# Optimization experiments

Measured on AMD Instinct MI355X. Metric: run time of the kernel, lower is better.

The kernel has to match this reference:

```python
import jax, jax.numpy as jnp
import numpy as np

B, T, N, D_IN = 2, 64, 64, 512
HID, L, H = 256, 2, 4
C = HID // H  # 64 per-head channels
NEG_SLOPE = 0.2
LN_EPS = 1e-5


def setup_inputs() -> dict:
    key = jax.random.key(0)
    ks = jax.random.split(key, 8)
    s_in = 1.0 / np.sqrt(D_IN)
    s_h = 1.0 / np.sqrt(HID)
    s_c = 1.0 / np.sqrt(C)
    return {
        "x": jax.random.normal(ks[0], (B, T, N, D_IN), jnp.float32),
        "person_mask": jax.random.randint(ks[1], (B, T, N), 0, 2) > 0,
        "W_in": (jax.random.normal(ks[2], (D_IN, HID)) * s_in).astype(jnp.float32),
        "b_in": jnp.zeros((HID,), jnp.float32),
        "Wl": (jax.random.normal(ks[3], (L, HID, HID)) * s_h).astype(jnp.float32),
        "bl": jnp.zeros((L, HID), jnp.float32),
        "Wr": (jax.random.normal(ks[4], (L, HID, HID)) * s_h).astype(jnp.float32),
        "br": jnp.zeros((L, HID), jnp.float32),
        "att": (jax.random.normal(ks[5], (L, H, C)) * s_c).astype(jnp.float32),
        "out_bias": jnp.zeros((L, HID), jnp.float32),
        "ln_scale": jnp.ones((L, HID), jnp.float32),
        "ln_bias": jnp.zeros((L, HID), jnp.float32),
    }


def _layernorm(x, g, b):
    mu = jnp.mean(x, axis=-1, keepdims=True)
    var = jnp.mean(jnp.square(x - mu), axis=-1, keepdims=True)
    return (x - mu) * jax.lax.rsqrt(var + LN_EPS) * g + b


def _gatv2_layer(h, allowed, Wl, bl, Wr, br, att, ob):
    # h: [bt, N, HID]; allowed: [bt, N, N] bool (edge j->i at [b,i,j])
    bt, n, _ = h.shape
    xl = (h @ Wl + bl).reshape(bt, n, H, C)  # source features (messages)
    xr = (h @ Wr + br).reshape(bt, n, H, C)  # target features
    # GATv2 logit: e_ij = a . leaky_relu(xr_i + xl_j), per head
    s = xr[:, :, None, :, :] + xl[:, None, :, :, :]  # [bt, i, j, H, C]
    e = jnp.einsum('bijhc,hc->bijh', jax.nn.leaky_relu(s, NEG_SLOPE), att)
    e = jnp.where(allowed[..., None], e, -1e9)
    alpha = jax.nn.softmax(e, axis=2)  # segment softmax over incoming edges j
    out = jnp.einsum('bijh,bjhc->bihc', alpha, xl)  # weighted scatter-sum
    return out.reshape(bt, n, H * C) + ob


def _forward(x, person_mask, W_in, b_in, Wl, bl, Wr, br, att, out_bias, ln_scale, ln_bias):
    b, t, n, _ = x.shape
    bt = b * t
    h = (x @ W_in + b_in).reshape(bt, n, HID)
    m = person_mask.reshape(bt, n)
    # edges: all pairs among masked nodes (incl. diag) + self loops for every node
    allowed = (m[:, :, None] & m[:, None, :]) | jnp.eye(n, dtype=bool)[None]
    hi = h
    for li in range(L):
        res = hi
        g = _gatv2_layer(hi, allowed, Wl[li], bl[li], Wr[li], br[li], att[li], out_bias[li])
        g = jax.nn.elu(g)  # dropout is identity in eval mode
        g = _layernorm(g, ln_scale[li], ln_bias[li])
        hi = g + res  # use_residual=True
        hi = jnp.where(m[:, :, None], hi, 0.0)
    # graphs with <=1 masked node are skipped (pass through projected features)
    keep = (jnp.sum(m, axis=-1) > 1)[:, None, None]
    out = jnp.where(keep, hi, h)
    return out.reshape(b, t, n, HID)


def reference(x, person_mask, W_in, b_in, Wl, bl, Wr, br, att, out_bias, ln_scale, ln_bias):
    return _forward(x, person_mask, W_in, b_in, Wl, bl, Wr, br, att, out_bias, ln_scale, ln_bias)
```

## Files before the change

### kernel.cpp

```cpp
#include <hip/hip_runtime.h>
#include <hip/hip_bf16.h>

#define BT_G   128
#define NND    64
#define D_IN_  512
#define HID_   256
#define NH     4
#define NCH    64
#define NROWS  8192
#define LN_EPS_    1e-5f

typedef __hip_bfloat16 bf16;
typedef __attribute__((ext_vector_type(8))) short short8;
typedef __attribute__((ext_vector_type(4))) float float4v;

__device__ __forceinline__ float toF(bf16 x) { return __bfloat162float(x); }

__global__ __launch_bounds__(256) void transpose_all_kernel(
    const float* __restrict__ W_in, const float* __restrict__ Wl,
    const float* __restrict__ Wr, const unsigned int* __restrict__ mw,
    bf16* __restrict__ WTin, bf16* __restrict__ WlrT, int* __restrict__ mout) {
    const int z = blockIdx.z;
    const int tid = threadIdx.x;
    if (z == 5) {
        if (blockIdx.x || blockIdx.y) return;
        __shared__ int okInt, okF32, okB16, okByte;
        if (tid == 0) { okInt = 1; okF32 = 1; okB16 = 1; okByte = 1; }
        __syncthreads();
        int aI = 1, aF = 1, aB = 1, aC = 1;
        for (int i = tid; i < 2048; i += 256) {
            unsigned w = mw[i];
            aI &= (w <= 1u);
            aF &= (w == 0u || w == 0x3F800000u);
            unsigned lo = w & 0xFFFFu, hi = w >> 16;
            aB &= ((lo == 0u || lo == 0x3F80u) && (hi == 0u || hi == 0x3F80u));
            aC &= (((w | (w >> 8) | (w >> 16) | (w >> 24)) & 0xFEu) == 0u);
        }
        if (!aI) atomicAnd(&okInt, 0);
        if (!aF) atomicAnd(&okF32, 0);
        if (!aB) atomicAnd(&okB16, 0);
        if (!aC) atomicAnd(&okByte, 0);
        __syncthreads();
        const int layout = (okInt || okF32) ? 0 : (okB16 ? 2 : (okByte ? 3 : 0));
        for (int i = tid; i < NROWS; i += 256) {
            int v;
            if (layout == 2)      v = (((const unsigned short*)mw)[i] != 0);
            else if (layout == 3) v = (((const unsigned char*)mw)[i] != 0);
            else                  v = (mw[i] != 0u);
            mout[i] = v;
        }
        return;
    }
    __shared__ float t[32][33];
    const float* src; bf16* dst; int K;
    if (z == 0)      { src = W_in;                 dst = WTin;                    K = 512; }
    else if (z <= 2) { src = Wl + (z - 1) * 65536; dst = WlrT + (z - 1) * 131072; K = 256; }
    else             { src = Wr + (z - 3) * 65536; dst = WlrT + (z - 3) * 131072 + 256 * 256; K = 256; }
    const int n0 = blockIdx.x * 32, k0 = blockIdx.y * 32;
    if (k0 >= K) return;
    const int tx = tid & 31, ty = tid >> 5;
    #pragma unroll
    for (int i = 0; i < 4; ++i)
        t[ty + 8 * i][tx] = src[(size_t)(k0 + ty + 8 * i) * 256 + n0 + tx];
    __syncthreads();
    #pragma unroll
    for (int i = 0; i < 4; ++i)
        dst[(size_t)(n0 + ty + 8 * i) * K + k0 + tx] =
            __float2bfloat16(t[tx][ty + 8 * i]);
}

__global__ __launch_bounds__(256) void gemm_in_kernel(
    const float* __restrict__ A, const bf16* __restrict__ BT,
    const float* __restrict__ bias, float* __restrict__ Cf,
    bf16* __restrict__ Cb16)
{
    __shared__ bf16 As[64 * 72];
    __shared__ bf16 Bs[64 * 72];
    const int tid  = threadIdx.x;
    const int wave = tid >> 6, lane = tid & 63;
    const int quad = lane >> 4, l16 = lane & 15;
    const int m0 = blockIdx.y * 64, n0 = blockIdx.x * 64;
    const int wm = (wave & 1) * 32, wn = (wave >> 1) * 32;
    float4v acc[2][2] = {};
    const int r  = tid >> 2;
    const int cq = (tid & 3) * 16;

    for (int k0 = 0; k0 < D_IN_; k0 += 64) {
        const float* sa = A + (size_t)(m0 + r) * D_IN_ + k0 + cq;
        const float4 f0 = *(const float4*)(sa);
        const float4 f1 = *(const float4*)(sa + 4);
        const float4 f2 = *(const float4*)(sa + 8);
        const float4 f3 = *(const float4*)(sa + 12);
        const bf16* sb = BT + (size_t)(n0 + r) * D_IN_ + k0 + cq;
        const float4 b0 = *(const float4*)(sb);
        const float4 b1 = *(const float4*)(sb + 8);
        union { bf16 h[16]; float4 v[2]; } u;
        u.h[0]=__float2bfloat16(f0.x); u.h[1]=__float2bfloat16(f0.y);
        u.h[2]=__float2bfloat16(f0.z); u.h[3]=__float2bfloat16(f0.w);
        u.h[4]=__float2bfloat16(f1.x); u.h[5]=__float2bfloat16(f1.y);
        u.h[6]=__float2bfloat16(f1.z); u.h[7]=__float2bfloat16(f1.w);
        u.h[8]=__float2bfloat16(f2.x); u.h[9]=__float2bfloat16(f2.y);
        u.h[10]=__float2bfloat16(f2.z); u.h[11]=__float2bfloat16(f2.w);
        u.h[12]=__float2bfloat16(f3.x); u.h[13]=__float2bfloat16(f3.y);
        u.h[14]=__float2bfloat16(f3.z); u.h[15]=__float2bfloat16(f3.w);
        __syncthreads();
        *(float4*)(&As[r * 72 + cq])     = u.v[0];
        *(float4*)(&As[r * 72 + cq + 8]) = u.v[1];
        *(float4*)(&Bs[r * 72 + cq])     = b0;
        *(float4*)(&Bs[r * 72 + cq + 8]) = b1;
        __syncthreads();
        #pragma unroll
        for (int kk = 0; kk < 64; kk += 32) {
            short8 af[2], bf2[2];
            #pragma unroll
            for (int mi = 0; mi < 2; ++mi)
                af[mi] = *(const short8*)(&As[(wm + mi * 16 + l16) * 72 + kk + quad * 8]);
            #pragma unroll
            for (int ni = 0; ni < 2; ++ni)
                bf2[ni] = *(const short8*)(&Bs[(wn + ni * 16 + l16) * 72 + kk + quad * 8]);
            #pragma unroll
            for (int mi = 0; mi < 2; ++mi)
                #pragma unroll
                for (int ni = 0; ni < 2; ++ni)
                    acc[mi][ni] = __builtin_amdgcn_mfma_f32_16x16x32_bf16(
                        af[mi], bf2[ni], acc[mi][ni], 0, 0, 0);
        }
    }
    #pragma unroll
    for (int ni = 0; ni < 2; ++ni) {
        const int col = n0 + wn + ni * 16 + l16;
        const float bv = bias[col];
        #pragma unroll
        for (int mi = 0; mi < 2; ++mi)
            #pragma unroll
            for (int rr = 0; rr < 4; ++rr) {
                const int row = m0 + wm + mi * 16 + quad * 4 + rr;
                const float v = acc[mi][ni][rr] + bv;
                Cf[(size_t)row * HID_ + col] = v;
                Cb16[(size_t)row * HID_ + col] = __float2bfloat16(v);
            }
    }
}

__global__ __launch_bounds__(256) void gemm_mfma_kernel(
    const bf16* __restrict__ A, const bf16* __restrict__ BT,
    const float* __restrict__ bias0, const float* __restrict__ bias1,
    float* __restrict__ Ca, float* __restrict__ Cbf, int M, int K)
{
    __shared__ bf16 As[128 * 72];
    __shared__ bf16 Bs[64 * 72];
    const int tid  = threadIdx.x;
    const int wave = tid >> 6, lane = tid & 63;
    const int quad = lane >> 4, l16 = lane & 15;
    const int m0 = blockIdx.y * 128, n0g = blockIdx.x * 64;
    const int wm = (wave & 1) * 64, wn = (wave >> 1) * 32;
    float4v acc[4][2] = {};
    const int r  = tid >> 2;
    const int cq = (tid & 3) * 16;

    for (int k0 = 0; k0 < K; k0 += 64) {
        const bf16* sa0 = A  + (size_t)(m0 + r) * K + k0 + cq;
        const bf16* sa1 = sa0 + (size_t)64 * K;
        const bf16* sb  = BT + (size_t)(n0g + r) * K + k0 + cq;
        const float4 a00 = *(const float4*)(sa0);
        const float4 a01 = *(const float4*)(sa0 + 8);
        const float4 a10 = *(const float4*)(sa1);
        const float4 a11 = *(const float4*)(sa1 + 8);
        const float4 b0  = *(const float4*)(sb);
        const float4 b1  = *(const float4*)(sb + 8);
        __syncthreads();
        *(float4*)(&As[r * 72 + cq])            = a00;
        *(float4*)(&As[r * 72 + cq + 8])        = a01;
        *(float4*)(&As[(r + 64) * 72 + cq])     = a10;
        *(float4*)(&As[(r + 64) * 72 + cq + 8]) = a11;
        *(float4*)(&Bs[r * 72 + cq])            = b0;
        *(float4*)(&Bs[r * 72 + cq + 8])        = b1;
        __syncthreads();
        #pragma unroll
        for (int kk = 0; kk < 64; kk += 32) {
            short8 af[4], bf2[2];
            #pragma unroll
            for (int mi = 0; mi < 4; ++mi)
                af[mi] = *(const short8*)(&As[(wm + mi * 16 + l16) * 72 + kk + quad * 8]);
            #pragma unroll
            for (int ni = 0; ni < 2; ++ni)
                bf2[ni] = *(const short8*)(&Bs[(wn + ni * 16 + l16) * 72 + kk + quad * 8]);
            #pragma unroll
            for (int mi = 0; mi < 4; ++mi)
                #pragma unroll
                for (int ni = 0; ni < 2; ++ni)
                    acc[mi][ni] = __builtin_amdgcn_mfma_f32_16x16x32_bf16(
                        af[mi], bf2[ni], acc[mi][ni], 0, 0, 0);
        }
    }
    const bool loHalf = (n0g < 256);
    float* Co = loHalf ? Ca : Cbf;
    const float* bp = loHalf ? bias0 : bias1;
    const int cbase = loHalf ? n0g : (n0g - 256);
    #pragma unroll
    for (int ni = 0; ni < 2; ++ni) {
        const int col = cbase + wn + ni * 16 + l16;
        const float bv = bp[col];
        #pragma unroll
        for (int mi = 0; mi < 4; ++mi)
            #pragma unroll
            for (int rr = 0; rr < 4; ++rr) {
                const int row = m0 + wm + mi * 16 + quad * 4 + rr;
                Co[(size_t)row * 256 + col] = acc[mi][ni][rr] + bv;
            }
    }
}

__global__ __launch_bounds__(256) void attn_kernel(
    const float* xl, const float* xr, const float* att,
    const int* msk, float* g)
{
    __shared__ float xls [64][68];
    __shared__ float xlsT[64][68];
    __shared__ float xrsT[64][68];
    __shared__ float esT [64][68];
    __shared__ float av[64], P[64], Q[64], mxf[64], inv[64];
    __shared__ float pmax[4][64], psum[4][64];
    __shared__ int   ms[64];
    const int tid  = threadIdx.x;
    const int head = blockIdx.x, gr = blockIdx.y;
    const int ti = tid >> 4, tj = tid & 15;
    const int i0 = ti * 4, j0 = tj * 4;
    const float* xlg = xl + (size_t)gr * NND * HID_ + head * NCH;
    const float* xrg = xr + (size_t)gr * NND * HID_ + head * NCH;

    {
        const int r  = tid >> 2;
        const int c0 = (tid & 3) * 16;
        float a[4][4], b[4][4];
        #pragma unroll
        for (int k = 0; k < 4; ++k) {
            *(float4*)a[k] = *(const float4*)(xlg + r * HID_ + c0 + 4 * k);
            *(float4*)b[k] = *(const float4*)(xrg + r * HID_ + c0 + 4 * k);
        }
        #pragma unroll
        for (int k = 0; k < 4; ++k)
            *(float4*)&xls[r][c0 + 4 * k] = *(float4*)a[k];
        #pragma unroll
        for (int k = 0; k < 4; ++k)
            #pragma unroll
            for (int w = 0; w < 4; ++w) {
                xlsT[c0 + 4 * k + w][r] = a[k][w];
                xrsT[c0 + 4 * k + w][r] = b[k][w];
            }
    }
    if (tid < 64) {
        av[tid] = att[head * NCH + tid];
        ms[tid] = msk[gr * NND + tid];
    }
    __syncthreads();

    float aa[4][4] = {};
    for (int c = 0; c < 64; ++c) {
        float xr4[4], xl4[4];
        *(float4*)xr4 = *(const float4*)&xrsT[c][i0];
        *(float4*)xl4 = *(const float4*)&xlsT[c][j0];
        const float a = av[c];
        #pragma unroll
        for (int y = 0; y < 4; ++y)
            #pragma unroll
            for (int x = 0; x < 4; ++x)
                aa[y][x] = fmaf(a, fabsf(xr4[y] + xl4[x]), aa[y][x]);
    }
    if (tid < 64) {
        float s = 0.f;
        for (int c = 0; c < 64; ++c) s = fmaf(av[c], xrsT[c][tid], s);
        P[tid] = s;
    } else if (tid < 128) {
        const int j = tid - 64;
        float s = 0.f;
        for (int c = 0; c < 64; ++c) s = fmaf(av[c], xlsT[c][j], s);
        Q[j] = s;
    }
    __syncthreads();

    {
        float Pv[4], Qv[4]; int mi4[4], mj4[4];
        #pragma unroll
        for (int y = 0; y < 4; ++y) { Pv[y] = P[i0 + y]; mi4[y] = ms[i0 + y]; }
        #pragma unroll
        for (int x = 0; x < 4; ++x) { Qv[x] = Q[j0 + x]; mj4[x] = ms[j0 + x]; }
        #pragma unroll
        for (int x = 0; x < 4; ++x) {
            float col[4];
            #pragma unroll
            for (int y = 0; y < 4; ++y) {
                float e = fmaf(0.4f, aa[y][x], 0.6f * (Pv[y] + Qv[x]));
                const bool allowed = (mi4[y] && mj4[x]) || (i0 + y == j0 + x);
                col[y] = allowed ? e : -1e9f;
            }
            *(float4*)&esT[j0 + x][i0] = *(float4*)col;
        }
    }
    __syncthreads();

    {
        const int si = tid & 63, q = tid >> 6;
        float mx = -1e30f;
        #pragma unroll
        for (int k = 0; k < 16; ++k) mx = fmaxf(mx, esT[16 * q + k][si]);
        pmax[q][si] = mx;
    }
    __syncthreads();
    if (tid < 64)
        mxf[tid] = fmaxf(fmaxf(pmax[0][tid], pmax[1][tid]),
                         fmaxf(pmax[2][tid], pmax[3][tid]));
    __syncthreads();
    {
        const int si = tid & 63, q = tid >> 6;
        const float mx = mxf[si];
        float s = 0.f;
        #pragma unroll
        for (int k = 0; k < 16; ++k) {
            const float ev = __expf(esT[16 * q + k][si] - mx);
            esT[16 * q + k][si] = ev;
            s += ev;
        }
        psum[q][si] = s;
    }
    __syncthreads();
    if (tid < 64)
        inv[tid] = 1.f / (psum[0][tid] + psum[1][tid] + psum[2][tid] + psum[3][tid]);
    __syncthreads();

    {
        const int c0 = j0;
        float oa[4][4] = {};
        for (int j = 0; j < 64; ++j) {
            float al[4], xv[4];
            *(float4*)al = *(const float4*)&esT[j][i0];
            *(float4*)xv = *(const float4*)&xls[j][c0];
            #pragma unroll
            for (int y = 0; y < 4; ++y)
                #pragma unroll
                for (int x = 0; x < 4; ++x)
                    oa[y][x] = fmaf(al[y], xv[x], oa[y][x]);
        }
        #pragma unroll
        for (int y = 0; y < 4; ++y) {
            const float iv = inv[i0 + y];
            float o[4];
            #pragma unroll
            for (int x = 0; x < 4; ++x) o[x] = oa[y][x] * iv;
            float* go = g + (size_t)(gr * NND + i0 + y) * HID_ + head * NCH + c0;
            *(float4*)go = *(float4*)o;
        }
    }
}

__global__ __launch_bounds__(256) void epilogue_kernel(
    const float* __restrict__ g, const float* res,
    const float* __restrict__ ob, const float* __restrict__ lns,
    const float* __restrict__ lnb, const int* __restrict__ msk,
    float* hout, bf16* hb, int finalSel)
{
    const int lane = threadIdx.x & 63;
    const int wave = threadIdx.x >> 6;
    const int m = blockIdx.x * 4 + wave;
    if (finalSel) {
        const int gr = m >> 6;
        const int mv = msk[gr * NND + lane];
        const unsigned long long bal = __ballot(mv != 0);
        if (__popcll(bal) <= 1) return;
    }
    const float* grow = g + (size_t)m * HID_;
    float v[4];
    float sum = 0.f;
    #pragma unroll
    for (int q = 0; q < 4; ++q) {
        const int c = q * 64 + lane;
        float x = grow[c] + ob[c];
        x = x > 0.f ? x : (__expf(x) - 1.f);
        v[q] = x; sum += x;
    }
    #pragma unroll
    for (int off = 1; off < 64; off <<= 1) sum += __shfl_xor(sum, off);
    const float mu = sum * (1.f / 256.f);
    float vs = 0.f;
    #pragma unroll
    for (int q = 0; q < 4; ++q) { const float d = v[q] - mu; vs += d * d; }
    #pragma unroll
    for (int off = 1; off < 64; off <<= 1) vs += __shfl_xor(vs, off);
    const float rstd = rsqrtf(vs * (1.f / 256.f) + LN_EPS_);
    const int mnode = msk[m];
    const float* rrow = res + (size_t)m * HID_;
    float* ho = hout + (size_t)m * HID_;
    #pragma unroll
    for (int q = 0; q < 4; ++q) {
        const int c = q * 64 + lane;
        float y = (v[q] - mu) * rstd * lns[c] + lnb[c];
        y += rrow[c];
        y = mnode ? y : 0.f;
        ho[c] = y;
        if (hb) hb[(size_t)m * HID_ + c] = __float2bfloat16(y);
    }
}

extern "C" void kernel_launch(void* const* d_in, const int* in_sizes, int n_in,
                              void* d_out, int out_size, void* d_ws, size_t ws_size,
                              hipStream_t stream) {
    const float* x    = (const float*)d_in[0];
    const float* W_in = (const float*)d_in[2];
    const float* b_in = (const float*)d_in[3];
    const float* Wl   = (const float*)d_in[4];
    const float* bl   = (const float*)d_in[5];
    const float* Wr   = (const float*)d_in[6];
    const float* br   = (const float*)d_in[7];
    const float* att  = (const float*)d_in[8];
    const float* ob   = (const float*)d_in[9];
    const float* lns  = (const float*)d_in[10];
    const float* lnb  = (const float*)d_in[11];
    float* out = (float*)d_out;

    char* w = (char*)d_ws;
    int*   mcan = (int*)w;                      w += 32768;
    float* h    = (float*)w;                    w += (size_t)NROWS * HID_ * 4;
    float* xlb  = (float*)w;                    w += (size_t)NROWS * HID_ * 4;
    float* xrb  = (float*)w;                    w += (size_t)NROWS * HID_ * 4;
    bf16*  hxb  = (bf16*)w;                     w += (size_t)NROWS * HID_ * 2;
    bf16*  WTin = (bf16*)w;                     w += (size_t)D_IN_ * HID_ * 2;
    bf16*  WlrT = (bf16*)w;
    float* gb   = xrb;

    transpose_all_kernel<<<dim3(8, 16, 6), 256, 0, stream>>>(
        W_in, Wl, Wr, (const unsigned int*)d_in[1], WTin, WlrT, mcan);

    gemm_in_kernel<<<dim3(HID_ / 64, NROWS / 64), 256, 0, stream>>>(
        x, WTin, b_in, out, hxb);

    for (int li = 0; li < 2; ++li) {
        const float* resf = (li == 0) ? out : h;
        gemm_mfma_kernel<<<dim3(512 / 64, NROWS / 128), 256, 0, stream>>>(
            hxb, WlrT + (size_t)li * 512 * HID_, bl + li * HID_, br + li * HID_,
            xlb, xrb, NROWS, HID_);
        attn_kernel<<<dim3(NH, BT_G), 256, 0, stream>>>(
            xlb, xrb, att + li * NH * NCH, mcan, gb);
        if (li == 0) {
            epilogue_kernel<<<NROWS / 4, 256, 0, stream>>>(
                gb, resf, ob, lns, lnb, mcan, h, hxb, 0);
        } else {
            epilogue_kernel<<<NROWS / 4, 256, 0, stream>>>(
                gb, resf, ob + HID_, lns + HID_, lnb + HID_, mcan,
                out, (bf16*)nullptr, 1);
        }
    }

    (void)in_sizes; (void)n_in; (void)out_size; (void)ws_size;
}
```

Measured before the change: 177.4 us.

## Fuse all stages into one persistent kernel with software grid barriers

Replaces the eight separate launches (weight transpose, input GEMM, two rounds of projection GEMM, attention and LN epilogue) with a single 512-block persistent kernel. Stages are separated by atomic-counter grid barriers and share an LDS union arena. This removes per-launch overhead and inter-kernel gaps. In exchange it needs all 512 blocks to be co-resident for the barriers to avoid deadlock, adds spin-wait barrier cost, and the large attention LDS arena may reduce occupancy.

```diff
diff --git a/kernel.cpp b/kernel.cpp
--- a/kernel.cpp
+++ b/kernel.cpp
@@ -9,395 +9,426 @@
 #define NCH    64
 #define NROWS  8192
 #define LN_EPS_    1e-5f
+#define NBLK   512
 
 typedef __hip_bfloat16 bf16;
 typedef __attribute__((ext_vector_type(8))) short short8;
 typedef __attribute__((ext_vector_type(4))) float float4v;
 
-__device__ __forceinline__ float toF(bf16 x) { return __bfloat162float(x); }
-
-__global__ __launch_bounds__(256) void transpose_all_kernel(
-    const float* __restrict__ W_in, const float* __restrict__ Wl,
-    const float* __restrict__ Wr, const unsigned int* __restrict__ mw,
-    bf16* __restrict__ WTin, bf16* __restrict__ WlrT, int* __restrict__ mout) {
-    const int z = blockIdx.z;
+__device__ __align__(64) int g_bar[16 * 16];
+
+__device__ __forceinline__ void grid_barrier(int p) {
+    __syncthreads();
+    if (threadIdx.x == 0) {
+        __threadfence();
+        const int old = __hip_atomic_fetch_add(&g_bar[p * 16], 1,
+                                               __ATOMIC_RELEASE,
+                                               __HIP_MEMORY_SCOPE_AGENT);
+        const int goal = ((old >> 9) << 9) + NBLK;
+        while (__hip_atomic_load(&g_bar[p * 16], __ATOMIC_ACQUIRE,
+                                 __HIP_MEMORY_SCOPE_AGENT) < goal)
+            __builtin_amdgcn_s_sleep(16);
+        __threadfence();
+    }
+    __syncthreads();
+}
+
+union Arena {
+    struct { float t[32][33]; } tr;
+    struct { int flags[4]; } mk;
+    struct { bf16 As[64 * 72]; bf16 Bs[64 * 72]; } gi;
+    struct { bf16 As[128 * 72]; bf16 Bs[64 * 72]; } gm;
+    struct {
+        float xls[64][68], xlsT[64][68], xrsT[64][68], esT[64][68];
+        float av[64], P[64], Q[64], mxf[64], inv[64];
+        float pmax[4][64], psum[4][64];
+        int   ms[64];
+    } at;
+};
+
+__global__ __launch_bounds__(256, 2) void mega_kernel(
+    const float* x, const unsigned* mw, const float* W_in, const float* b_in,
+    const float* Wl, const float* bl, const float* Wr, const float* br,
+    const float* att, const float* ob, const float* lns, const float* lnb,
+    float* out, int* mcan, float* h, float* xlb, float* xrb,
+    bf16* hxb, bf16* WTin, bf16* WlrT)
+{
+    __shared__ Arena ar;
     const int tid = threadIdx.x;
-    if (z == 5) {
-        if (blockIdx.x || blockIdx.y) return;
-        __shared__ int okInt, okF32, okB16, okByte;
-        if (tid == 0) { okInt = 1; okF32 = 1; okB16 = 1; okByte = 1; }
+    const int bid = blockIdx.x;
+
+    if (bid < 384) {
+        int z, xb, yb;
+        if (bid < 128) { z = 0; xb = bid & 7; yb = bid >> 3; }
+        else { const int q = bid - 128; z = 1 + (q >> 6);
+               const int s = q & 63; xb = s & 7; yb = s >> 3; }
+        const float* src; bf16* dst; int K;
+        if (z == 0)      { src = W_in;                 dst = WTin;                         K = 512; }
+        else if (z <= 2) { src = Wl + (z - 1) * 65536; dst = WlrT + (z - 1) * 131072;      K = 256; }
+        else             { src = Wr + (z - 3) * 65536; dst = WlrT + (z - 3) * 131072 + 65536; K = 256; }
+        const int n0 = xb * 32, k0 = yb * 32;
+        const int tx = tid & 31, ty = tid >> 5;
+        #pragma unroll
+        for (int i = 0; i < 4; ++i)
+            ar.tr.t[ty + 8 * i][tx] = src[(size_t)(k0 + ty + 8 * i) * 256 + n0 + tx];
+        __syncthreads();
+        #pragma unroll
+        for (int i = 0; i < 4; ++i)
+            dst[(size_t)(n0 + ty + 8 * i) * K + k0 + tx] =
+                __float2bfloat16(ar.tr.t[tx][ty + 8 * i]);
+    } else if (bid == 384) {
+        int* fl = ar.mk.flags;
+        if (tid == 0) { fl[0] = 1; fl[1] = 1; fl[2] = 1; fl[3] = 1; }
         __syncthreads();
         int aI = 1, aF = 1, aB = 1, aC = 1;
         for (int i = tid; i < 2048; i += 256) {
-            unsigned w = mw[i];
-            aI &= (w <= 1u);
-            aF &= (w == 0u || w == 0x3F800000u);
-            unsigned lo = w & 0xFFFFu, hi = w >> 16;
+            const unsigned w2 = mw[i];
+            aI &= (w2 <= 1u);
+            aF &= (w2 == 0u || w2 == 0x3F800000u);
+            const unsigned lo = w2 & 0xFFFFu, hi = w2 >> 16;
             aB &= ((lo == 0u || lo == 0x3F80u) && (hi == 0u || hi == 0x3F80u));
-            aC &= (((w | (w >> 8) | (w >> 16) | (w >> 24)) & 0xFEu) == 0u);
-        }
-        if (!aI) atomicAnd(&okInt, 0);
-        if (!aF) atomicAnd(&okF32, 0);
-        if (!aB) atomicAnd(&okB16, 0);
-        if (!aC) atomicAnd(&okByte, 0);
+            aC &= (((w2 | (w2 >> 8) | (w2 >> 16) | (w2 >> 24)) & 0xFEu) == 0u);
+        }
+        if (!aI) atomicAnd(&fl[0], 0);
+        if (!aF) atomicAnd(&fl[1], 0);
+        if (!aB) atomicAnd(&fl[2], 0);
+        if (!aC) atomicAnd(&fl[3], 0);
         __syncthreads();
-        const int layout = (okInt || okF32) ? 0 : (okB16 ? 2 : (okByte ? 3 : 0));
+        const int layout = (fl[0] || fl[1]) ? 0 : (fl[2] ? 2 : (fl[3] ? 3 : 0));
         for (int i = tid; i < NROWS; i += 256) {
             int v;
             if (layout == 2)      v = (((const unsigned short*)mw)[i] != 0);
             else if (layout == 3) v = (((const unsigned char*)mw)[i] != 0);
             else                  v = (mw[i] != 0u);
-            mout[i] = v;
-        }
-        return;
+            mcan[i] = v;
+        }
     }
-    __shared__ float t[32][33];
-    const float* src; bf16* dst; int K;
-    if (z == 0)      { src = W_in;                 dst = WTin;                    K = 512; }
-    else if (z <= 2) { src = Wl + (z - 1) * 65536; dst = WlrT + (z - 1) * 131072; K = 256; }
-    else             { src = Wr + (z - 3) * 65536; dst = WlrT + (z - 3) * 131072 + 256 * 256; K = 256; }
-    const int n0 = blockIdx.x * 32, k0 = blockIdx.y * 32;
-    if (k0 >= K) return;
-    const int tx = tid & 31, ty = tid >> 5;
-    #pragma unroll
-    for (int i = 0; i < 4; ++i)
-        t[ty + 8 * i][tx] = src[(size_t)(k0 + ty + 8 * i) * 256 + n0 + tx];
-    __syncthreads();
-    #pragma unroll
-    for (int i = 0; i < 4; ++i)
-        dst[(size_t)(n0 + ty + 8 * i) * K + k0 + tx] =
-            __float2bfloat16(t[tx][ty + 8 * i]);
-}
-
-__global__ __launch_bounds__(256) void gemm_in_kernel(
-    const float* __restrict__ A, const bf16* __restrict__ BT,
-    const float* __restrict__ bias, float* __restrict__ Cf,
-    bf16* __restrict__ Cb16)
-{
-    __shared__ bf16 As[64 * 72];
-    __shared__ bf16 Bs[64 * 72];
-    const int tid  = threadIdx.x;
-    const int wave = tid >> 6, lane = tid & 63;
-    const int quad = lane >> 4, l16 = lane & 15;
-    const int m0 = blockIdx.y * 64, n0 = blockIdx.x * 64;
-    const int wm = (wave & 1) * 32, wn = (wave >> 1) * 32;
-    float4v acc[2][2] = {};
-    const int r  = tid >> 2;
-    const int cq = (tid & 3) * 16;
-
-    for (int k0 = 0; k0 < D_IN_; k0 += 64) {
-        const float* sa = A + (size_t)(m0 + r) * D_IN_ + k0 + cq;
-        const float4 f0 = *(const float4*)(sa);
-        const float4 f1 = *(const float4*)(sa + 4);
-        const float4 f2 = *(const float4*)(sa + 8);
-        const float4 f3 = *(const float4*)(sa + 12);
-        const bf16* sb = BT + (size_t)(n0 + r) * D_IN_ + k0 + cq;
-        const float4 b0 = *(const float4*)(sb);
-        const float4 b1 = *(const float4*)(sb + 8);
-        union { bf16 h[16]; float4 v[2]; } u;
-        u.h[0]=__float2bfloat16(f0.x); u.h[1]=__float2bfloat16(f0.y);
-        u.h[2]=__float2bfloat16(f0.z); u.h[3]=__float2bfloat16(f0.w);
-        u.h[4]=__float2bfloat16(f1.x); u.h[5]=__float2bfloat16(f1.y);
-        u.h[6]=__float2bfloat16(f1.z); u.h[7]=__float2bfloat16(f1.w);
-        u.h[8]=__float2bfloat16(f2.x); u.h[9]=__float2bfloat16(f2.y);
-        u.h[10]=__float2bfloat16(f2.z); u.h[11]=__float2bfloat16(f2.w);
-        u.h[12]=__float2bfloat16(f3.x); u.h[13]=__float2bfloat16(f3.y);
-        u.h[14]=__float2bfloat16(f3.z); u.h[15]=__float2bfloat16(f3.w);
-        __syncthreads();
-        *(float4*)(&As[r * 72 + cq])     = u.v[0];
-        *(float4*)(&As[r * 72 + cq + 8]) = u.v[1];
-        *(float4*)(&Bs[r * 72 + cq])     = b0;
-        *(float4*)(&Bs[r * 72 + cq + 8]) = b1;
-        __syncthreads();
+    grid_barrier(0);
+
+    {
+        bf16* As = ar.gi.As;
+        bf16* Bs = ar.gi.Bs;
+        const int wave = tid >> 6, lane = tid & 63;
+        const int quad = lane >> 4, l16 = lane & 15;
+        const int m0 = (bid >> 2) * 64, n0 = (bid & 3) * 64;
+        const int wm = (wave & 1) * 32, wn = (wave >> 1) * 32;
+        float4v acc[2][2] = {};
+        const int r  = tid >> 2;
+        const int cq = (tid & 3) * 16;
+        for (int k0 = 0; k0 < D_IN_; k0 += 64) {
+            const float* sa = x + (size_t)(m0 + r) * D_IN_ + k0 + cq;
+            const float4 f0 = *(const float4*)(sa);
+            const float4 f1 = *(const float4*)(sa + 4);
+            const float4 f2 = *(const float4*)(sa + 8);
+            const float4 f3 = *(const float4*)(sa + 12);
+            const bf16* sb = WTin + (size_t)(n0 + r) * D_IN_ + k0 + cq;
+            const float4 b0 = *(const float4*)(sb);
+            const float4 b1 = *(const float4*)(sb + 8);
+            union { bf16 hh[16]; float4 v[2]; } u;
+            u.hh[0]=__float2bfloat16(f0.x); u.hh[1]=__float2bfloat16(f0.y);
+            u.hh[2]=__float2bfloat16(f0.z); u.hh[3]=__float2bfloat16(f0.w);
+            u.hh[4]=__float2bfloat16(f1.x); u.hh[5]=__float2bfloat16(f1.y);
+            u.hh[6]=__float2bfloat16(f1.z); u.hh[7]=__float2bfloat16(f1.w);
+            u.hh[8]=__float2bfloat16(f2.x); u.hh[9]=__float2bfloat16(f2.y);
+            u.hh[10]=__float2bfloat16(f2.z); u.hh[11]=__float2bfloat16(f2.w);
+            u.hh[12]=__float2bfloat16(f3.x); u.hh[13]=__float2bfloat16(f3.y);
+            u.hh[14]=__float2bfloat16(f3.z); u.hh[15]=__float2bfloat16(f3.w);
+            __syncthreads();
+            *(float4*)(&As[r * 72 + cq])     = u.v[0];
+            *(float4*)(&As[r * 72 + cq + 8]) = u.v[1];
+            *(float4*)(&Bs[r * 72 + cq])     = b0;
+            *(float4*)(&Bs[r * 72 + cq + 8]) = b1;
+            __syncthreads();
+            #pragma unroll
+            for (int kk = 0; kk < 64; kk += 32) {
+                short8 af[2], bf2[2];
+                #pragma unroll
+                for (int mi = 0; mi < 2; ++mi)
+                    af[mi] = *(const short8*)(&As[(wm + mi * 16 + l16) * 72 + kk + quad * 8]);
+                #pragma unroll
+                for (int ni = 0; ni < 2; ++ni)
+                    bf2[ni] = *(const short8*)(&Bs[(wn + ni * 16 + l16) * 72 + kk + quad * 8]);
+                #pragma unroll
+                for (int mi = 0; mi < 2; ++mi)
+                    #pragma unroll
+                    for (int ni = 0; ni < 2; ++ni)
+                        acc[mi][ni] = __builtin_amdgcn_mfma_f32_16x16x32_bf16(
+                            af[mi], bf2[ni], acc[mi][ni], 0, 0, 0);
+            }
+        }
         #pragma unroll
-        for (int kk = 0; kk < 64; kk += 32) {
-            short8 af[2], bf2[2];
+        for (int ni = 0; ni < 2; ++ni) {
+            const int col = n0 + wn + ni * 16 + l16;
+            const float bv = b_in[col];
             #pragma unroll
             for (int mi = 0; mi < 2; ++mi)
-                af[mi] = *(const short8*)(&As[(wm + mi * 16 + l16) * 72 + kk + quad * 8]);
+                #pragma unroll
+                for (int rr = 0; rr < 4; ++rr) {
+                    const int row = m0 + wm + mi * 16 + quad * 4 + rr;
+                    const float v = acc[mi][ni][rr] + bv;
+                    out[(size_t)row * HID_ + col] = v;
+                    hxb[(size_t)row * HID_ + col] = __float2bfloat16(v);
+                }
+        }
+    }
+    grid_barrier(1);
+
+    for (int li = 0; li < 2; ++li) {
+        {
+            bf16* As = ar.gm.As;
+            bf16* Bs = ar.gm.Bs;
+            const bf16* BT = WlrT + (size_t)li * 512 * HID_;
+            const float* bias0 = bl + li * HID_;
+            const float* bias1 = br + li * HID_;
+            const int wave = tid >> 6, lane = tid & 63;
+            const int quad = lane >> 4, l16 = lane & 15;
+            const int m0 = (bid >> 3) * 128, n0g = (bid & 7) * 64;
+            const int wm = (wave & 1) * 64, wn = (wave >> 1) * 32;
+            float4v acc[4][2] = {};
+            const int r  = tid >> 2;
+            const int cq = (tid & 3) * 16;
+            for (int k0 = 0; k0 < HID_; k0 += 64) {
+                const bf16* sa0 = hxb + (size_t)(m0 + r) * HID_ + k0 + cq;
+                const bf16* sa1 = sa0 + (size_t)64 * HID_;
+                const bf16* sb  = BT + (size_t)(n0g + r) * HID_ + k0 + cq;
+                const float4 a00 = *(const float4*)(sa0);
+                const float4 a01 = *(const float4*)(sa0 + 8);
+                const float4 a10 = *(const float4*)(sa1);
+                const float4 a11 = *(const float4*)(sa1 + 8);
+                const float4 b0  = *(const float4*)(sb);
+                const float4 b1  = *(const float4*)(sb + 8);
+                __syncthreads();
+                *(float4*)(&As[r * 72 + cq])            = a00;
+                *(float4*)(&As[r * 72 + cq + 8])        = a01;
+                *(float4*)(&As[(r + 64) * 72 + cq])     = a10;
+                *(float4*)(&As[(r + 64) * 72 + cq + 8]) = a11;
+                *(float4*)(&Bs[r * 72 + cq])            = b0;
+                *(float4*)(&Bs[r * 72 + cq + 8])        = b1;
+                __syncthreads();
+                #pragma unroll
+                for (int kk = 0; kk < 64; kk += 32) {
+                    short8 af[4], bf2[2];
+                    #pragma unroll
+                    for (int mi = 0; mi < 4; ++mi)
+                        af[mi] = *(const short8*)(&As[(wm + mi * 16 + l16) * 72 + kk + quad * 8]);
+                    #pragma unroll
+                    for (int ni = 0; ni < 2; ++ni)
+                        bf2[ni] = *(const short8*)(&Bs[(wn + ni * 16 + l16) * 72 + kk + quad * 8]);
+                    #pragma unroll
+                    for (int mi = 0; mi < 4; ++mi)
+                        #pragma unroll
+                        for (int ni = 0; ni < 2; ++ni)
+                            acc[mi][ni] = __builtin_amdgcn_mfma_f32_16x16x32_bf16(
+                                af[mi], bf2[ni], acc[mi][ni], 0, 0, 0);
+                }
+            }
+            const bool loHalf = (n0g < 256);
+            float* Co = loHalf ? xlb : xrb;
+            const float* bp = loHalf ? bias0 : bias1;
+            const int cbase = loHalf ? n0g : (n0g - 256);
             #pragma unroll
-            for (int ni = 0; ni < 2; ++ni)
-                bf2[ni] = *(const short8*)(&Bs[(wn + ni * 16 + l16) * 72 + kk + quad * 8]);
-            #pragma unroll
-            for (int mi = 0; mi < 2; ++mi)
-                #pragma unroll
-                for (int ni = 0; ni < 2; ++ni)
-                    acc[mi][ni] = __builtin_amdgcn_mfma_f32_16x16x32_bf16(
-                        af[mi], bf2[ni], acc[mi][ni], 0, 0, 0);
-        }
-    }
-    #pragma unroll
-    for (int ni = 0; ni < 2; ++ni) {
-        const int col = n0 + wn + ni * 16 + l16;
-        const float bv = bias[col];
-        #pragma unroll
-        for (int mi = 0; mi < 2; ++mi)
-            #pragma unroll
-            for (int rr = 0; rr < 4; ++rr) {
-                const int row = m0 + wm + mi * 16 + quad * 4 + rr;
-                const float v = acc[mi][ni][rr] + bv;
-                Cf[(size_t)row * HID_ + col] = v;
-                Cb16[(size_t)row * HID_ + col] = __float2bfloat16(v);
-            }
-    }
-}
-
-__global__ __launch_bounds__(256) void gemm_mfma_kernel(
-    const bf16* __restrict__ A, const bf16* __restrict__ BT,
-    const float* __restrict__ bias0, const float* __restrict__ bias1,
-    float* __restrict__ Ca, float* __restrict__ Cbf, int M, int K)
-{
-    __shared__ bf16 As[128 * 72];
-    __shared__ bf16 Bs[64 * 72];
-    const int tid  = threadIdx.x;
-    const int wave = tid >> 6, lane = tid & 63;
-    const int quad = lane >> 4, l16 = lane & 15;
-    const int m0 = blockIdx.y * 128, n0g = blockIdx.x * 64;
-    const int wm = (wave & 1) * 64, wn = (wave >> 1) * 32;
-    float4v acc[4][2] = {};
-    const int r  = tid >> 2;
-    const int cq = (tid & 3) * 16;
-
-    for (int k0 = 0; k0 < K; k0 += 64) {
-        const bf16* sa0 = A  + (size_t)(m0 + r) * K + k0 + cq;
-        const bf16* sa1 = sa0 + (size_t)64 * K;
-        const bf16* sb  = BT + (size_t)(n0g + r) * K + k0 + cq;
-        const float4 a00 = *(const float4*)(sa0);
-        const float4 a01 = *(const float4*)(sa0 + 8);
-        const float4 a10 = *(const float4*)(sa1);
-        const float4 a11 = *(const float4*)(sa1 + 8);
-        const float4 b0  = *(const float4*)(sb);
-        const float4 b1  = *(const float4*)(sb + 8);
-        __syncthreads();
-        *(float4*)(&As[r * 72 + cq])            = a00;
-        *(float4*)(&As[r * 72 + cq + 8])        = a01;
-        *(float4*)(&As[(r + 64) * 72 + cq])     = a10;
-        *(float4*)(&As[(r + 64) * 72 + cq + 8]) = a11;
-        *(float4*)(&Bs[r * 72 + cq])            = b0;
-        *(float4*)(&Bs[r * 72 + cq + 8])        = b1;
-        __syncthreads();
-        #pragma unroll
-        for (int kk = 0; kk < 64; kk += 32) {
-            short8 af[4], bf2[2];
-            #pragma unroll
-            for (int mi = 0; mi < 4; ++mi)
-                af[mi] = *(const short8*)(&As[(wm + mi * 16 + l16) * 72 + kk + quad * 8]);
-            #pragma unroll
-            for (int ni = 0; ni < 2; ++ni)
-                bf2[ni] = *(const short8*)(&Bs[(wn + ni * 16 + l16) * 72 + kk + quad * 8]);
-            #pragma unroll
-            for (int mi = 0; mi < 4; ++mi)
-                #pragma unroll
-                for (int ni = 0; ni < 2; ++ni)
-                    acc[mi][ni] = __builtin_amdgcn_mfma_f32_16x16x32_bf16(
-                        af[mi], bf2[ni], acc[mi][ni], 0, 0, 0);
-        }
-    }
-    const bool loHalf = (n0g < 256);
-    float* Co = loHalf ? Ca : Cbf;
-    const float* bp = loHalf ? bias0 : bias1;
-    const int cbase = loHalf ? n0g : (n0g - 256);
-    #pragma unroll
-    for (int ni = 0; ni < 2; ++ni) {
-        const int col = cbase + wn + ni * 16 + l16;
-        const float bv = bp[col];
-        #pragma unroll
-        for (int mi = 0; mi < 4; ++mi)
-            #pragma unroll
-            for (int rr = 0; rr < 4; ++rr) {
-                const int row = m0 + wm + mi * 16 + quad * 4 + rr;
-                Co[(size_t)row * 256 + col] = acc[mi][ni][rr] + bv;
-            }
-    }
-}
-
-__global__ __launch_bounds__(256) void attn_kernel(
-    const float* xl, const float* xr, const float* att,
-    const int* msk, float* g)
-{
-    __shared__ float xls [64][68];
-    __shared__ float xlsT[64][68];
-    __shared__ float xrsT[64][68];
-    __shared__ float esT [64][68];
-    __shared__ float av[64], P[64], Q[64], mxf[64], inv[64];
-    __shared__ float pmax[4][64], psum[4][64];
-    __shared__ int   ms[64];
-    const int tid  = threadIdx.x;
-    const int head = blockIdx.x, gr = blockIdx.y;
-    const int ti = tid >> 4, tj = tid & 15;
-    const int i0 = ti * 4, j0 = tj * 4;
-    const float* xlg = xl + (size_t)gr * NND * HID_ + head * NCH;
-    const float* xrg = xr + (size_t)gr * NND * HID_ + head * NCH;
-
-    {
-        const int r  = tid >> 2;
-        const int c0 = (tid & 3) * 16;
-        float a[4][4], b[4][4];
-        #pragma unroll
-        for (int k = 0; k < 4; ++k) {
-            *(float4*)a[k] = *(const float4*)(xlg + r * HID_ + c0 + 4 * k);
-            *(float4*)b[k] = *(const float4*)(xrg + r * HID_ + c0 + 4 * k);
-        }
-        #pragma unroll
-        for (int k = 0; k < 4; ++k)
-            *(float4*)&xls[r][c0 + 4 * k] = *(float4*)a[k];
-        #pragma unroll
-        for (int k = 0; k < 4; ++k)
-            #pragma unroll
-            for (int w = 0; w < 4; ++w) {
-                xlsT[c0 + 4 * k + w][r] = a[k][w];
-                xrsT[c0 + 4 * k + w][r] = b[k][w];
-            }
-    }
-    if (tid < 64) {
-        av[tid] = att[head * NCH + tid];
-        ms[tid] = msk[gr * NND + tid];
-    }
-    __syncthreads();
-
-    float aa[4][4] = {};
-    for (int c = 0; c < 64; ++c) {
-        float xr4[4], xl4[4];
-        *(float4*)xr4 = *(const float4*)&xrsT[c][i0];
-        *(float4*)xl4 = *(const float4*)&xlsT[c][j0];
-        const float a = av[c];
-        #pragma unroll
-        for (int y = 0; y < 4; ++y)
-            #pragma unroll
-            for (int x = 0; x < 4; ++x)
-                aa[y][x] = fmaf(a, fabsf(xr4[y] + xl4[x]), aa[y][x]);
-    }
-    if (tid < 64) {
-        float s = 0.f;
-        for (int c = 0; c < 64; ++c) s = fmaf(av[c], xrsT[c][tid], s);
-        P[tid] = s;
-    } else if (tid < 128) {
-        const int j = tid - 64;
-        float s = 0.f;
-        for (int c = 0; c < 64; ++c) s = fmaf(av[c], xlsT[c][j], s);
-        Q[j] = s;
-    }
-    __syncthreads();
-
-    {
-        float Pv[4], Qv[4]; int mi4[4], mj4[4];
-        #pragma unroll
-        for (int y = 0; y < 4; ++y) { Pv[y] = P[i0 + y]; mi4[y] = ms[i0 + y]; }
-        #pragma unroll
-        for (int x = 0; x < 4; ++x) { Qv[x] = Q[j0 + x]; mj4[x] = ms[j0 + x]; }
-        #pragma unroll
-        for (int x = 0; x < 4; ++x) {
-            float col[4];
-            #pragma unroll
-            for (int y = 0; y < 4; ++y) {
-                float e = fmaf(0.4f, aa[y][x], 0.6f * (Pv[y] + Qv[x]));
-                const bool allowed = (mi4[y] && mj4[x]) || (i0 + y == j0 + x);
-                col[y] = allowed ? e : -1e9f;
-            }
-            *(float4*)&esT[j0 + x][i0] = *(float4*)col;
-        }
-    }
-    __syncthreads();
-
-    {
-        const int si = tid & 63, q = tid >> 6;
-        float mx = -1e30f;
-        #pragma unroll
-        for (int k = 0; k < 16; ++k) mx = fmaxf(mx, esT[16 * q + k][si]);
-        pmax[q][si] = mx;
-    }
-    __syncthreads();
-    if (tid < 64)
-        mxf[tid] = fmaxf(fmaxf(pmax[0][tid], pmax[1][tid]),
-                         fmaxf(pmax[2][tid], pmax[3][tid]));
-    __syncthreads();
-    {
-        const int si = tid & 63, q = tid >> 6;
-        const float mx = mxf[si];
-        float s = 0.f;
-        #pragma unroll
-        for (int k = 0; k < 16; ++k) {
-            const float ev = __expf(esT[16 * q + k][si] - mx);
-            esT[16 * q + k][si] = ev;
-            s += ev;
-        }
-        psum[q][si] = s;
-    }
-    __syncthreads();
-    if (tid < 64)
-        inv[tid] = 1.f / (psum[0][tid] + psum[1][tid] + psum[2][tid] + psum[3][tid]);
-    __syncthreads();
-
-    {
-        const int c0 = j0;
-        float oa[4][4] = {};
-        for (int j = 0; j < 64; ++j) {
-            float al[4], xv[4];
-            *(float4*)al = *(const float4*)&esT[j][i0];
-            *(float4*)xv = *(const float4*)&xls[j][c0];
-            #pragma unroll
-            for (int y = 0; y < 4; ++y)
-                #pragma unroll
-                for (int x = 0; x < 4; ++x)
-                    oa[y][x] = fmaf(al[y], xv[x], oa[y][x]);
-        }
-        #pragma unroll
-        for (int y = 0; y < 4; ++y) {
-            const float iv = inv[i0 + y];
-            float o[4];
-            #pragma unroll
-            for (int x = 0; x < 4; ++x) o[x] = oa[y][x] * iv;
-            float* go = g + (size_t)(gr * NND + i0 + y) * HID_ + head * NCH + c0;
-            *(float4*)go = *(float4*)o;
-        }
-    }
-}
-
-__global__ __launch_bounds__(256) void epilogue_kernel(
-    const float* __restrict__ g, const float* res,
-    const float* __restrict__ ob, const float* __restrict__ lns,
-    const float* __restrict__ lnb, const int* __restrict__ msk,
-    float* hout, bf16* hb, int finalSel)
-{
-    const int lane = threadIdx.x & 63;
-    const int wave = threadIdx.x >> 6;
-    const int m = blockIdx.x * 4 + wave;
-    if (finalSel) {
-        const int gr = m >> 6;
-        const int mv = msk[gr * NND + lane];
-        const unsigned long long bal = __ballot(mv != 0);
-        if (__popcll(bal) <= 1) return;
-    }
-    const float* grow = g + (size_t)m * HID_;
-    float v[4];
-    float sum = 0.f;
-    #pragma unroll
-    for (int q = 0; q < 4; ++q) {
-        const int c = q * 64 + lane;
-        float x = grow[c] + ob[c];
-        x = x > 0.f ? x : (__expf(x) - 1.f);
-        v[q] = x; sum += x;
-    }
-    #pragma unroll
-    for (int off = 1; off < 64; off <<= 1) sum += __shfl_xor(sum, off);
-    const float mu = sum * (1.f / 256.f);
-    float vs = 0.f;
-    #pragma unroll
-    for (int q = 0; q < 4; ++q) { const float d = v[q] - mu; vs += d * d; }
-    #pragma unroll
-    for (int off = 1; off < 64; off <<= 1) vs += __shfl_xor(vs, off);
-    const float rstd = rsqrtf(vs * (1.f / 256.f) + LN_EPS_);
-    const int mnode = msk[m];
-    const float* rrow = res + (size_t)m * HID_;
-    float* ho = hout + (size_t)m * HID_;
-    #pragma unroll
-    for (int q = 0; q < 4; ++q) {
-        const int c = q * 64 + lane;
-        float y = (v[q] - mu) * rstd * lns[c] + lnb[c];
-        y += rrow[c];
-        y = mnode ? y : 0.f;
-        ho[c] = y;
-        if (hb) hb[(size_t)m * HID_ + c] = __float2bfloat16(y);
+            for (int ni = 0; ni < 2; ++ni) {
+                const int col = cbase + wn + ni * 16 + l16;
+                const float bv = bp[col];
+                #pragma unroll
+                for (int mi = 0; mi < 4; ++mi)
+                    #pragma unroll
+                    for (int rr = 0; rr < 4; ++rr) {
+                        const int row = m0 + wm + mi * 16 + quad * 4 + rr;
+                        Co[(size_t)row * 256 + col] = acc[mi][ni][rr] + bv;
+                    }
+            }
+        }
+        grid_barrier(2 + li * 3);
+
+        {
+            auto& A = ar.at;
+            const int head = bid & 3, gr = bid >> 2;
+            const float* attp = att + li * NH * NCH;
+            float* g = xrb;
+            const int ti = tid >> 4, tj = tid & 15;
+            const int i0 = ti * 4, j0 = tj * 4;
+            const float* xlg = xlb + (size_t)gr * NND * HID_ + head * NCH;
+            const float* xrg = xrb + (size_t)gr * NND * HID_ + head * NCH;
+            {
+                const int r  = tid >> 2;
+                const int c0 = (tid & 3) * 16;
+                float a[4][4], b[4][4];
+                #pragma unroll
+                for (int k = 0; k < 4; ++k) {
+                    *(float4*)a[k] = *(const float4*)(xlg + r * HID_ + c0 + 4 * k);
+                    *(float4*)b[k] = *(const float4*)(xrg + r * HID_ + c0 + 4 * k);
+                }
+                #pragma unroll
+                for (int k = 0; k < 4; ++k)
+                    *(float4*)&A.xls[r][c0 + 4 * k] = *(float4*)a[k];
+                #pragma unroll
+                for (int k = 0; k < 4; ++k)
+                    #pragma unroll
+                    for (int w = 0; w < 4; ++w) {
+                        A.xlsT[c0 + 4 * k + w][r] = a[k][w];
+                        A.xrsT[c0 + 4 * k + w][r] = b[k][w];
+                    }
+            }
+            if (tid < 64) {
+                A.av[tid] = attp[head * NCH + tid];
+                A.ms[tid] = mcan[gr * NND + tid];
+            }
+            __syncthreads();
+
+            float aa[4][4] = {};
+            for (int c = 0; c < 64; ++c) {
+                float xr4[4], xl4[4];
+                *(float4*)xr4 = *(const float4*)&A.xrsT[c][i0];
+                *(float4*)xl4 = *(const float4*)&A.xlsT[c][j0];
+                const float a = A.av[c];
+                #pragma unroll
+                for (int y = 0; y < 4; ++y)
+                    #pragma unroll
+                    for (int xx = 0; xx < 4; ++xx)
+                        aa[y][xx] = fmaf(a, fabsf(xr4[y] + xl4[xx]), aa[y][xx]);
+            }
+            if (tid < 64) {
+                float s = 0.f;
+                for (int c = 0; c < 64; ++c) s = fmaf(A.av[c], A.xrsT[c][tid], s);
+                A.P[tid] = s;
+            } else if (tid < 128) {
+                const int j = tid - 64;
+                float s = 0.f;
+                for (int c = 0; c < 64; ++c) s = fmaf(A.av[c], A.xlsT[c][j], s);
+                A.Q[j] = s;
+            }
+            __syncthreads();
+
+            {
+                float Pv[4], Qv[4]; int mi4[4], mj4[4];
+                #pragma unroll
+                for (int y = 0; y < 4; ++y) { Pv[y] = A.P[i0 + y]; mi4[y] = A.ms[i0 + y]; }
+                #pragma unroll
+                for (int xx = 0; xx < 4; ++xx) { Qv[xx] = A.Q[j0 + xx]; mj4[xx] = A.ms[j0 + xx]; }
+                #pragma unroll
+                for (int xx = 0; xx < 4; ++xx) {
+                    float col[4];
+                    #pragma unroll
+                    for (int y = 0; y < 4; ++y) {
+                        float e = fmaf(0.4f, aa[y][xx], 0.6f * (Pv[y] + Qv[xx]));
+                        const bool allowed = (mi4[y] && mj4[xx]) || (i0 + y == j0 + xx);
+                        col[y] = allowed ? e : -1e9f;
+                    }
+                    *(float4*)&A.esT[j0 + xx][i0] = *(float4*)col;
+                }
+            }
+            __syncthreads();
+
+            {
+                const int si = tid & 63, q = tid >> 6;
+                float mx = -1e30f;
+                #pragma unroll
+                for (int k = 0; k < 16; ++k) mx = fmaxf(mx, A.esT[16 * q + k][si]);
+                A.pmax[q][si] = mx;
+            }
+            __syncthreads();
+            if (tid < 64)
+                A.mxf[tid] = fmaxf(fmaxf(A.pmax[0][tid], A.pmax[1][tid]),
+                                   fmaxf(A.pmax[2][tid], A.pmax[3][tid]));
+            __syncthreads();
+            {
+                const int si = tid & 63, q = tid >> 6;
+                const float mx = A.mxf[si];
+                float s = 0.f;
+                #pragma unroll
+                for (int k = 0; k < 16; ++k) {
+                    const float ev = __expf(A.esT[16 * q + k][si] - mx);
+                    A.esT[16 * q + k][si] = ev;
+                    s += ev;
+                }
+                A.psum[q][si] = s;
+            }
+            __syncthreads();
+            if (tid < 64)
+                A.inv[tid] = 1.f / (A.psum[0][tid] + A.psum[1][tid] +
+                                    A.psum[2][tid] + A.psum[3][tid]);
+            __syncthreads();
+
+            {
+                const int c0 = j0;
+                float oa[4][4] = {};
+                for (int j = 0; j < 64; ++j) {
+                    float al[4], xv[4];
+                    *(float4*)al = *(const float4*)&A.esT[j][i0];
+                    *(float4*)xv = *(const float4*)&A.xls[j][c0];
+                    #pragma unroll
+                    for (int y = 0; y < 4; ++y)
+                        #pragma unroll
+                        for (int xx = 0; xx < 4; ++xx)
+                            oa[y][xx] = fmaf(al[y], xv[xx], oa[y][xx]);
+                }
+                #pragma unroll
+                for (int y = 0; y < 4; ++y) {
+                    const float iv = A.inv[i0 + y];
+                    float o[4];
+                    #pragma unroll
+                    for (int xx = 0; xx < 4; ++xx) o[xx] = oa[y][xx] * iv;
+                    float* go = g + (size_t)(gr * NND + i0 + y) * HID_ + head * NCH + c0;
+                    *(float4*)go = *(float4*)o;
+                }
+            }
+        }
+        grid_barrier(3 + li * 3);
+
+        {
+            const float* gsrc = xrb;
+            const float* resf = (li == 0) ? out : h;
+            float* hout = (li == 0) ? h : out;
+            bf16* hb = (li == 0) ? hxb : (bf16*)nullptr;
+            const float* obp  = ob  + li * HID_;
+            const float* lnsp = lns + li * HID_;
+            const float* lnbp = lnb + li * HID_;
+            const int lane = tid & 63, wv = tid >> 6;
+            for (int t4 = 0; t4 < 4; ++t4) {
+                const int m = (bid << 4) + (t4 << 2) + wv;
+                bool doit = true;
+                if (li == 1) {
+                    const int gr = m >> 6;
+                    const unsigned long long bal = __ballot(mcan[gr * NND + lane] != 0);
+                    doit = (__popcll(bal) > 1);
+                }
+                if (doit) {
+                    const float* grow = gsrc + (size_t)m * HID_;
+                    float v[4];
+                    float sum = 0.f;
+                    #pragma unroll
+                    for (int q = 0; q < 4; ++q) {
+                        const int c = q * 64 + lane;
+                        float xv = grow[c] + obp[c];
+                        xv = xv > 0.f ? xv : (__expf(xv) - 1.f);
+                        v[q] = xv; sum += xv;
+                    }
+                    #pragma unroll
+                    for (int off = 1; off < 64; off <<= 1) sum += __shfl_xor(sum, off);
+                    const float mu = sum * (1.f / 256.f);
+                    float vs = 0.f;
+                    #pragma unroll
+                    for (int q = 0; q < 4; ++q) { const float d = v[q] - mu; vs += d * d; }
+                    #pragma unroll
+                    for (int off = 1; off < 64; off <<= 1) vs += __shfl_xor(vs, off);
+                    const float rstd = rsqrtf(vs * (1.f / 256.f) + LN_EPS_);
+                    const int mnode = mcan[m];
+                    const float* rrow = resf + (size_t)m * HID_;
+                    float* ho = hout + (size_t)m * HID_;
+                    #pragma unroll
+                    for (int q = 0; q < 4; ++q) {
+                        const int c = q * 64 + lane;
+                        float y = (v[q] - mu) * rstd * lnsp[c] + lnbp[c];
+                        y += rrow[c];
+                        y = mnode ? y : 0.f;
+                        ho[c] = y;
+                        if (hb) hb[(size_t)m * HID_ + c] = __float2bfloat16(y);
+                    }
+                }
+            }
+        }
+        if (li == 0) grid_barrier(4);
     }
 }
 
@@ -425,30 +456,10 @@
     bf16*  hxb  = (bf16*)w;                     w += (size_t)NROWS * HID_ * 2;
     bf16*  WTin = (bf16*)w;                     w += (size_t)D_IN_ * HID_ * 2;
     bf16*  WlrT = (bf16*)w;
-    float* gb   = xrb;
-
-    transpose_all_kernel<<<dim3(8, 16, 6), 256, 0, stream>>>(
-        W_in, Wl, Wr, (const unsigned int*)d_in[1], WTin, WlrT, mcan);
-
-    gemm_in_kernel<<<dim3(HID_ / 64, NROWS / 64), 256, 0, stream>>>(
-        x, WTin, b_in, out, hxb);
-
-    for (int li = 0; li < 2; ++li) {
-        const float* resf = (li == 0) ? out : h;
-        gemm_mfma_kernel<<<dim3(512 / 64, NROWS / 128), 256, 0, stream>>>(
-            hxb, WlrT + (size_t)li * 512 * HID_, bl + li * HID_, br + li * HID_,
-            xlb, xrb, NROWS, HID_);
-        attn_kernel<<<dim3(NH, BT_G), 256, 0, stream>>>(
-            xlb, xrb, att + li * NH * NCH, mcan, gb);
-        if (li == 0) {
-            epilogue_kernel<<<NROWS / 4, 256, 0, stream>>>(
-                gb, resf, ob, lns, lnb, mcan, h, hxb, 0);
-        } else {
-            epilogue_kernel<<<NROWS / 4, 256, 0, stream>>>(
-                gb, resf, ob + HID_, lns + HID_, lnb + HID_, mcan,
-                out, (bf16*)nullptr, 1);
-        }
-    }
+
+    mega_kernel<<<NBLK, 256, 0, stream>>>(
+        x, (const unsigned*)d_in[1], W_in, b_in, Wl, bl, Wr, br,
+        att, ob, lns, lnb, out, mcan, h, xlb, xrb, hxb, WTin, WlrT);
 
     (void)in_sizes; (void)n_in; (void)out_size; (void)ws_size;
 }
```

New measurement: 688.6 us. 288% more time.
